# Kernel tuning notes

Hardware: AMD Instinct MI355X
Metric: run time of the kernel (lower is better)

## Reference

```python
import jax, jax.numpy as jnp
import numpy as np

SCALING = 32.0 / 16.0  # alpha / rank


def _nf4_levels():
    # q_i = Phi^{-1}((i+0.5)/16), normalized to [-1, 1]
    i = jnp.arange(16, dtype=jnp.float32)
    p = jnp.clip((i + 0.5) / 16.0, 1e-6, 1.0 - 1e-6)
    lv = jnp.sqrt(2.0) * jax.scipy.special.erfinv(2.0 * p - 1.0)
    return lv / jnp.max(jnp.abs(lv))


def _dequantize(q_weight, scales):
    # q_weight: (out, in//2) packed nibbles; scales: (out, num_groups)
    out_f, packed = q_weight.shape
    in_f = packed * 2
    hi = (q_weight >> 4) & 15
    lo = q_weight & 15
    idx = jnp.stack([hi, lo], axis=-1).reshape(out_f, in_f)  # interleave hi/lo
    w = _nf4_levels()[idx]  # (out, in)
    num_groups = scales.shape[1]
    block = in_f // num_groups
    w = (w.reshape(out_f, num_groups, block) * scales[:, :, None].astype(jnp.float32))
    return w.reshape(out_f, in_f)


def setup_inputs() -> dict:
    key = jax.random.key(0)
    k1, k2, k3, k4, k5 = jax.random.split(key, 5)
    B, S, IN, OUT, R, BLK = 4, 64, 8192, 8192, 16, 64
    x = jax.random.normal(k1, (B, S, IN), dtype=jnp.float32)
    q_weight = jax.random.randint(k2, (OUT, IN // 2), 0, 256, dtype=jnp.int32)
    scales = jax.random.uniform(k3, (OUT, IN // BLK), dtype=jnp.float32) * 0.02 + 1e-4
    lora_A = jax.random.normal(k4, (R, IN), dtype=jnp.float32) * 0.02
    lora_B = jax.random.normal(k5, (OUT, R), dtype=jnp.float32) * 0.02
    return {"x": x, "q_weight": q_weight, "scales": scales,
            "lora_A": lora_A, "lora_B": lora_B}


def reference(x, q_weight, scales, lora_A, lora_B):
    w = _dequantize(q_weight, scales)               # (out, in) fp32
    base = jnp.einsum('bsi,oi->bso', x, w)          # F.linear(x, W)
    lora = jnp.einsum('bsi,ri->bsr', x, lora_A)     # x @ A^T (dropout p=0)
    lora = jnp.einsum('bsr,or->bso', lora, lora_B)  # @ B^T
    return base + SCALING * lora
```

## Files before the change

kernel.cpp:

```cpp
#include <hip/hip_runtime.h>
#include <hip/hip_bf16.h>
#include <stdint.h>

typedef __attribute__((ext_vector_type(4))) float f32x4;
typedef __attribute__((ext_vector_type(8))) short short8;
typedef __attribute__((ext_vector_type(4))) int int4v;

#define IN_F   8192
#define OUT_F  8192
#define MROWS  256
#define BN     128
#define BK     64
#define NGRP   128

__device__ unsigned short g_xb[MROWS * IN_F];
__device__ float          g_t[MROWS * 16];
__device__ float          g_part[4 * MROWS * OUT_F];

__device__ __constant__ float NF4_LVL[16] = {
  -1.0f,        -0.70756721f, -0.54221982f, -0.41681853f,
  -0.31090474f, -0.21594601f, -0.12734085f, -0.04209530f,
   0.04209530f,  0.12734085f,  0.21594601f,  0.31090474f,
   0.41681853f,  0.54221982f,  0.70756721f,  1.0f };

static __device__ inline uint32_t pkbf(float a, float b) {
  __bf16 ha = (__bf16)a, hb = (__bf16)b;
  return (uint32_t)__builtin_bit_cast(unsigned short, ha)
       | ((uint32_t)__builtin_bit_cast(unsigned short, hb) << 16);
}

__global__ __launch_bounds__(256) void k_convert(const float* __restrict__ x) {
  int cid = blockIdx.x * 256 + threadIdx.x;
  int kt = cid >> 11;
  int r  = (cid >> 3) & 255;
  int c  = cid & 7;
  const float* src = x + (size_t)r * IN_F + kt * 64 + c * 8;
  f32x4 v0 = *(const f32x4*)src;
  f32x4 v1 = *(const f32x4*)(src + 4);
  int4v ov;
  ov[0] = (int)pkbf(v0.x, v0.y); ov[1] = (int)pkbf(v0.z, v0.w);
  ov[2] = (int)pkbf(v1.x, v1.y); ov[3] = (int)pkbf(v1.z, v1.w);
  *(int4v*)(g_xb + (size_t)kt * 16384 + r * 64 + ((c ^ (r & 7)) << 3)) = ov;
}

__global__ __launch_bounds__(256) void k_xa(const float* __restrict__ x,
                                            const float* __restrict__ lora_A) {
  int m = blockIdx.x, tid = threadIdx.x;
  float acc[16];
#pragma unroll
  for (int r = 0; r < 16; ++r) acc[r] = 0.f;
  const float* xr = x + (size_t)m * IN_F;
  for (int it = 0; it < 8; ++it) {
    int k = (tid + it * 256) * 4;
    f32x4 xv = *(const f32x4*)(xr + k);
#pragma unroll
    for (int r = 0; r < 16; ++r) {
      f32x4 av = *(const f32x4*)(lora_A + (size_t)r * IN_F + k);
      acc[r] += xv.x * av.x + xv.y * av.y + xv.z * av.z + xv.w * av.w;
    }
  }
#pragma unroll
  for (int r = 0; r < 16; ++r) {
    float v = acc[r];
#pragma unroll
    for (int off = 32; off; off >>= 1) v += __shfl_xor(v, off, 64);
    acc[r] = v;
  }
  __shared__ float sm[4][16];
  int lane = tid & 63, wave = tid >> 6;
  if (lane == 0) {
#pragma unroll
    for (int r = 0; r < 16; ++r) sm[wave][r] = acc[r];
  }
  __syncthreads();
  if (tid < 16)
    g_t[m * 16 + tid] = 2.0f * (sm[0][tid] + sm[1][tid] + sm[2][tid] + sm[3][tid]);
}

__global__ __launch_bounds__(512, 2) void k_gemm(
    const int* __restrict__ qw, const float* __restrict__ scales)
{
  __shared__ unsigned short Al[2][MROWS * BK];
  __shared__ unsigned short Bl[2][BN * BK];
  __shared__ float lut16[16];

  int tid = threadIdx.x;
  int lane = tid & 63, wave = tid >> 6;
  if (tid < 16) lut16[tid] = NF4_LVL[tid];
  __syncthreads();

  int flat = blockIdx.y * 64 + blockIdx.x;
  int wg = (flat & 7) * 32 + (flat >> 3);
  int bx = wg & 63, bz = wg >> 6;
  int n0 = bx * BN;
  int ktg0 = bz * 32;

  int n_0 = tid >> 3, c_0 = tid & 7;
  int n_1 = n_0 + 64;
  const int* qr0 = qw + (size_t)(n0 + n_0) * (IN_F / 2) + c_0 * 4;
  const int* qr1 = qw + (size_t)(n0 + n_1) * (IN_F / 2) + c_0 * 4;
  const float* sr0 = scales + (size_t)(n0 + n_0) * NGRP;
  const float* sr1 = scales + (size_t)(n0 + n_1) * NGRP;
  int boff0 = n_0 * 128 + ((c_0 ^ (n_0 & 7)) << 4);
  int boff1 = boff0 + 64 * 128;

  f32x4 acc[4][4];
#pragma unroll
  for (int i = 0; i < 4; ++i)
#pragma unroll
    for (int j = 0; j < 4; ++j) acc[i][j] = (f32x4){0.f, 0.f, 0.f, 0.f};

  int wr = wave >> 1, wc = wave & 1;
  int wm = wr * 64, wn = wc * 64;

  auto stageA = [&](int buf, int kt) {
    const char* src = (const char*)g_xb + (size_t)kt * 32768 + tid * 16;
    char* dst = (char*)(&Al[buf][0]) + tid * 16;
#pragma unroll
    for (int j = 0; j < 4; ++j)
      __builtin_amdgcn_global_load_lds(
          (const __attribute__((address_space(1))) void*)(src + j * 8192),
          (__attribute__((address_space(3))) void*)(dst + j * 8192), 16, 0, 0);
  };

  auto dqst = [&](int buf, int4v q0, float s0, int4v q1, float s1) {
    char* Bb = (char*)(&Bl[buf][0]);
    int4v ov;
#pragma unroll
    for (int e = 0; e < 4; ++e) {
      float hi = lut16[(q0[e] >> 4) & 15];
      float lo = lut16[q0[e] & 15];
      ov[e] = (int)pkbf(hi * s0, lo * s0);
    }
    *(int4v*)(Bb + boff0) = ov;
#pragma unroll
    for (int e = 0; e < 4; ++e) {
      float hi = lut16[(q1[e] >> 4) & 15];
      float lo = lut16[q1[e] & 15];
      ov[e] = (int)pkbf(hi * s1, lo * s1);
    }
    *(int4v*)(Bb + boff1) = ov;
  };

  auto compute = [&](int buf) {
    const char* Ab = (const char*)(&Al[buf][0]);
    const char* Bb = (const char*)(&Bl[buf][0]);
#pragma unroll
    for (int kk = 0; kk < 2; ++kk) {
      short8 af[4], bfv[4];
#pragma unroll
      for (int mi = 0; mi < 4; ++mi) {
        int r = wm + mi * 16 + (lane & 15);
        int cch = (kk * 4 + (lane >> 4)) ^ (r & 7);
        af[mi] = *(const short8*)(Ab + r * 128 + cch * 16);
      }
#pragma unroll
      for (int ni = 0; ni < 4; ++ni) {
        int n = wn + ni * 16 + (lane & 15);
        int cch = (kk * 4 + (lane >> 4)) ^ (n & 7);
        bfv[ni] = *(const short8*)(Bb + n * 128 + cch * 16);
      }
      __builtin_amdgcn_s_setprio(1);
#pragma unroll
      for (int mi = 0; mi < 4; ++mi)
#pragma unroll
        for (int ni = 0; ni < 4; ++ni)
          acc[mi][ni] = __builtin_amdgcn_mfma_f32_16x16x32_bf16(
              af[mi], bfv[ni], acc[mi][ni], 0, 0, 0);
      __builtin_amdgcn_s_setprio(0);
    }
  };

  int4v qa0 = *(const int4v*)(qr0 + ktg0 * 32);
  int4v qa1 = *(const int4v*)(qr1 + ktg0 * 32);
  float sa0 = sr0[ktg0], sa1 = sr1[ktg0];
  stageA(0, ktg0);
  int4v qb0 = *(const int4v*)(qr0 + (ktg0 + 1) * 32);
  int4v qb1 = *(const int4v*)(qr1 + (ktg0 + 1) * 32);
  float sb0 = sr0[ktg0 + 1], sb1 = sr1[ktg0 + 1];
  dqst(0, qa0, sa0, qa1, sa1);
  asm volatile("s_waitcnt vmcnt(0) lgkmcnt(0)" ::: "memory");
  __builtin_amdgcn_s_barrier();

  for (int t = 0; t < 31; ++t) {
    int c = t & 1;
    int kn = ktg0 + ((t < 30) ? (t + 2) : 0);
    int4v qn0 = *(const int4v*)(qr0 + kn * 32);
    int4v qn1 = *(const int4v*)(qr1 + kn * 32);
    float sn0 = sr0[kn], sn1 = sr1[kn];
    stageA(c ^ 1, ktg0 + t + 1);
    dqst(c ^ 1, qb0, sb0, qb1, sb1);
    compute(c);
    asm volatile("s_waitcnt vmcnt(0) lgkmcnt(0)" ::: "memory");
    __builtin_amdgcn_s_barrier();
    qb0 = qn0; qb1 = qn1; sb0 = sn0; sb1 = sn1;
  }
  compute(1);

  float* op = g_part + (size_t)bz * MROWS * OUT_F;
#pragma unroll
  for (int mi = 0; mi < 4; ++mi) {
#pragma unroll
    for (int ni = 0; ni < 4; ++ni) {
      int m = wm + mi * 16 + (lane >> 4) * 4;
      int nn = n0 + wn + ni * 16 + (lane & 15);
#pragma unroll
      for (int j = 0; j < 4; ++j)
        op[(size_t)(m + j) * OUT_F + nn] = acc[mi][ni][j];
    }
  }
}

__global__ __launch_bounds__(256) void k_reduce(const float* __restrict__ lora_B,
                                                float* __restrict__ out) {
  size_t i = ((size_t)blockIdx.x * 256 + threadIdx.x) * 4;
  int m = (int)(i >> 13);
  int n = (int)(i & 8191);
  f32x4 v = *(const f32x4*)(g_part + i);
  v += *(const f32x4*)(g_part + (size_t)1 * MROWS * OUT_F + i);
  v += *(const f32x4*)(g_part + (size_t)2 * MROWS * OUT_F + i);
  v += *(const f32x4*)(g_part + (size_t)3 * MROWS * OUT_F + i);
  const float* tr = g_t + m * 16;
  f32x4 t0 = *(const f32x4*)tr,       t1 = *(const f32x4*)(tr + 4);
  f32x4 t2 = *(const f32x4*)(tr + 8), t3 = *(const f32x4*)(tr + 12);
#pragma unroll
  for (int j = 0; j < 4; ++j) {
    const float* br = lora_B + (size_t)(n + j) * 16;
    f32x4 b0 = *(const f32x4*)br,       b1 = *(const f32x4*)(br + 4);
    f32x4 b2 = *(const f32x4*)(br + 8), b3 = *(const f32x4*)(br + 12);
    v[j] += t0.x*b0.x + t0.y*b0.y + t0.z*b0.z + t0.w*b0.w
          + t1.x*b1.x + t1.y*b1.y + t1.z*b1.z + t1.w*b1.w
          + t2.x*b2.x + t2.y*b2.y + t2.z*b2.z + t2.w*b2.w
          + t3.x*b3.x + t3.y*b3.y + t3.z*b3.z + t3.w*b3.w;
  }
  *(f32x4*)(out + i) = v;
}

extern "C" void kernel_launch(void* const* d_in, const int* in_sizes, int n_in,
                              void* d_out, int out_size, void* d_ws, size_t ws_size,
                              hipStream_t stream) {
  const float* x  = (const float*)d_in[0];
  const int*   qw = (const int*)d_in[1];
  const float* sc = (const float*)d_in[2];
  const float* lA = (const float*)d_in[3];
  const float* lB = (const float*)d_in[4];
  float* out = (float*)d_out;

  k_convert<<<1024, 256, 0, stream>>>(x);
  k_xa<<<256, 256, 0, stream>>>(x, lA);
  k_gemm<<<dim3(64, 4), 512, 0, stream>>>(qw, sc);
  k_reduce<<<2048, 256, 0, stream>>>(lB, out);
}
```

Before: 107.5 us.

## Pre-swizzle activations into MFMA fragment order and read them directly from global

k_convert now writes the bf16 activations in the exact per-lane MFMA fragment order, so the GEMM loads A operands straight from global (L2) into registers and drops the LDS staging of A. The N tile is halved to 64, giving 512 workgroups with launch bounds of 4 per CU, and LDS holds only the dequantized B tile. Dequantization uses a 256-entry LUT of packed bf16 pairs, so one lookup covers both nibbles of a byte. The intent is to cut LDS traffic and footprint and to raise occupancy and parallelism, at the cost of more redundant global reads of A across N tiles and higher latency on those A loads.

Result: no change. 107.1 us (-0.3%).

```diff
diff --git a/kernel.cpp b/kernel.cpp
--- a/kernel.cpp
+++ b/kernel.cpp
@@ -9,9 +9,10 @@
 #define IN_F   8192
 #define OUT_F  8192
 #define MROWS  256
-#define BN     128
+#define BN     64
 #define BK     64
 #define NGRP   128
+#define KTILES 32
 
 __device__ unsigned short g_xb[MROWS * IN_F];
 __device__ float          g_t[MROWS * 16];
@@ -30,17 +31,18 @@
 }
 
 __global__ __launch_bounds__(256) void k_convert(const float* __restrict__ x) {
-  int cid = blockIdx.x * 256 + threadIdx.x;
-  int kt = cid >> 11;
-  int r  = (cid >> 3) & 255;
-  int c  = cid & 7;
-  const float* src = x + (size_t)r * IN_F + kt * 64 + c * 8;
+  int d = blockIdx.x * 256 + threadIdx.x;
+  int l15 = d & 15, sub = (d >> 4) & 3, kk = (d >> 6) & 1;
+  int m16 = (d >> 7) & 15, kt = d >> 11;
+  int r = m16 * 16 + l15;
+  int k = kt * 64 + (kk * 4 + sub) * 8;
+  const float* src = x + (size_t)r * IN_F + k;
   f32x4 v0 = *(const f32x4*)src;
   f32x4 v1 = *(const f32x4*)(src + 4);
   int4v ov;
   ov[0] = (int)pkbf(v0.x, v0.y); ov[1] = (int)pkbf(v0.z, v0.w);
   ov[2] = (int)pkbf(v1.x, v1.y); ov[3] = (int)pkbf(v1.z, v1.w);
-  *(int4v*)(g_xb + (size_t)kt * 16384 + r * 64 + ((c ^ (r & 7)) << 3)) = ov;
+  *(int4v*)(g_xb + (size_t)d * 8) = ov;
 }
 
 __global__ __launch_bounds__(256) void k_xa(const float* __restrict__ x,
@@ -77,133 +79,141 @@
     g_t[m * 16 + tid] = 2.0f * (sm[0][tid] + sm[1][tid] + sm[2][tid] + sm[3][tid]);
 }
 
-__global__ __launch_bounds__(512, 2) void k_gemm(
+__global__ __launch_bounds__(512, 4) void k_gemm(
     const int* __restrict__ qw, const float* __restrict__ scales)
 {
-  __shared__ unsigned short Al[2][MROWS * BK];
   __shared__ unsigned short Bl[2][BN * BK];
-  __shared__ float lut16[16];
+  __shared__ uint32_t lut2[256];
 
   int tid = threadIdx.x;
   int lane = tid & 63, wave = tid >> 6;
-  if (tid < 16) lut16[tid] = NF4_LVL[tid];
+  if (tid < 256) lut2[tid] = pkbf(NF4_LVL[tid >> 4], NF4_LVL[tid & 15]);
+
+  int flat = blockIdx.x;
+  int wg = (flat & 7) * 64 + (flat >> 3);
+  int bx = wg & 127, bz = wg >> 7;
+  int n0 = bx * BN;
+  int ktg0 = bz * KTILES;
+
+  int dn = tid >> 3, dc = tid & 7;
+  const int* qr = qw + (size_t)(n0 + dn) * (IN_F / 2) + dc * 4;
+  const float* sr = scales + (size_t)(n0 + dn) * NGRP;
+  int boff = dn * 128 + ((dc ^ (dn & 7)) << 4);
+
+  f32x4 acc[4][2];
+#pragma unroll
+  for (int i = 0; i < 4; ++i)
+#pragma unroll
+    for (int j = 0; j < 2; ++j) acc[i][j] = (f32x4){0.f, 0.f, 0.f, 0.f};
+
+  int wr = wave >> 1, wc = wave & 1;
+  int wn = wc * 32;
+  int sub = lane >> 4, l15 = lane & 15;
+
+  int aoff = (wr * 4) * 1024 + (sub * 16 + l15) * 8;
+
+  auto dqst = [&](int buf, int4v q, float s) {
+    int4v ov;
+#pragma unroll
+    for (int e = 0; e < 4; ++e) {
+      uint32_t pk = lut2[q[e] & 255];
+      float fh = __builtin_bit_cast(float, pk << 16);
+      float fl = __builtin_bit_cast(float, pk & 0xFFFF0000u);
+      ov[e] = (int)pkbf(fh * s, fl * s);
+    }
+    *(int4v*)((char*)(&Bl[buf][0]) + boff) = ov;
+  };
+
   __syncthreads();
 
-  int flat = blockIdx.y * 64 + blockIdx.x;
-  int wg = (flat & 7) * 32 + (flat >> 3);
-  int bx = wg & 63, bz = wg >> 6;
-  int n0 = bx * BN;
-  int ktg0 = bz * 32;
-
-  int n_0 = tid >> 3, c_0 = tid & 7;
-  int n_1 = n_0 + 64;
-  const int* qr0 = qw + (size_t)(n0 + n_0) * (IN_F / 2) + c_0 * 4;
-  const int* qr1 = qw + (size_t)(n0 + n_1) * (IN_F / 2) + c_0 * 4;
-  const float* sr0 = scales + (size_t)(n0 + n_0) * NGRP;
-  const float* sr1 = scales + (size_t)(n0 + n_1) * NGRP;
-  int boff0 = n_0 * 128 + ((c_0 ^ (n_0 & 7)) << 4);
-  int boff1 = boff0 + 64 * 128;
-
-  f32x4 acc[4][4];
-#pragma unroll
-  for (int i = 0; i < 4; ++i)
-#pragma unroll
-    for (int j = 0; j < 4; ++j) acc[i][j] = (f32x4){0.f, 0.f, 0.f, 0.f};
-
-  int wr = wave >> 1, wc = wave & 1;
-  int wm = wr * 64, wn = wc * 64;
-
-  auto stageA = [&](int buf, int kt) {
-    const char* src = (const char*)g_xb + (size_t)kt * 32768 + tid * 16;
-    char* dst = (char*)(&Al[buf][0]) + tid * 16;
-#pragma unroll
-    for (int j = 0; j < 4; ++j)
-      __builtin_amdgcn_global_load_lds(
-          (const __attribute__((address_space(1))) void*)(src + j * 8192),
-          (__attribute__((address_space(3))) void*)(dst + j * 8192), 16, 0, 0);
-  };
-
-  auto dqst = [&](int buf, int4v q0, float s0, int4v q1, float s1) {
-    char* Bb = (char*)(&Bl[buf][0]);
-    int4v ov;
-#pragma unroll
-    for (int e = 0; e < 4; ++e) {
-      float hi = lut16[(q0[e] >> 4) & 15];
-      float lo = lut16[q0[e] & 15];
-      ov[e] = (int)pkbf(hi * s0, lo * s0);
-    }
-    *(int4v*)(Bb + boff0) = ov;
-#pragma unroll
-    for (int e = 0; e < 4; ++e) {
-      float hi = lut16[(q1[e] >> 4) & 15];
-      float lo = lut16[q1[e] & 15];
-      ov[e] = (int)pkbf(hi * s1, lo * s1);
-    }
-    *(int4v*)(Bb + boff1) = ov;
-  };
-
-  auto compute = [&](int buf) {
-    const char* Ab = (const char*)(&Al[buf][0]);
-    const char* Bb = (const char*)(&Bl[buf][0]);
-#pragma unroll
-    for (int kk = 0; kk < 2; ++kk) {
-      short8 af[4], bfv[4];
-#pragma unroll
-      for (int mi = 0; mi < 4; ++mi) {
-        int r = wm + mi * 16 + (lane & 15);
-        int cch = (kk * 4 + (lane >> 4)) ^ (r & 7);
-        af[mi] = *(const short8*)(Ab + r * 128 + cch * 16);
+  int4v qcur = *(const int4v*)(qr + ktg0 * 32);
+  float scur = sr[ktg0];
+  dqst(0, qcur, scur);
+  int4v qnxt = *(const int4v*)(qr + (ktg0 + 1) * 32);
+  float snxt = sr[ktg0 + 1];
+  asm volatile("s_waitcnt lgkmcnt(0)" ::: "memory");
+  __builtin_amdgcn_s_barrier();
+
+  for (int t = 0; t < KTILES - 1; ++t) {
+    int cur = t & 1;
+    int ktg = ktg0 + t;
+
+    short8 bfv[2][2];
+#pragma unroll
+    for (int kk = 0; kk < 2; ++kk)
+#pragma unroll
+      for (int ni = 0; ni < 2; ++ni) {
+        int n = wn + ni * 16 + l15;
+        int cch = (kk * 4 + sub) ^ (n & 7);
+        bfv[kk][ni] = *(const short8*)((const char*)(&Bl[cur][0]) + n * 128 + cch * 16);
       }
-#pragma unroll
-      for (int ni = 0; ni < 4; ++ni) {
-        int n = wn + ni * 16 + (lane & 15);
-        int cch = (kk * 4 + (lane >> 4)) ^ (n & 7);
-        bfv[ni] = *(const short8*)(Bb + n * 128 + cch * 16);
+
+    short8 af[2][4];
+    const unsigned short* ab = g_xb + (size_t)ktg * 16384;
+#pragma unroll
+    for (int kk = 0; kk < 2; ++kk)
+#pragma unroll
+      for (int mi = 0; mi < 4; ++mi)
+        af[kk][mi] = *(const short8*)(ab + aoff + mi * 1024 + kk * 512);
+
+    int kn = (t < KTILES - 2) ? (ktg0 + t + 2) : (ktg0 + KTILES - 1);
+    int4v qn2 = *(const int4v*)(qr + kn * 32);
+    float sn2 = sr[kn];
+
+    dqst(cur ^ 1, qnxt, snxt);
+    qnxt = qn2; snxt = sn2;
+
+    __builtin_amdgcn_s_setprio(1);
+#pragma unroll
+    for (int kk = 0; kk < 2; ++kk)
+#pragma unroll
+      for (int mi = 0; mi < 4; ++mi)
+#pragma unroll
+        for (int ni = 0; ni < 2; ++ni)
+          acc[mi][ni] = __builtin_amdgcn_mfma_f32_16x16x32_bf16(
+              af[kk][mi], bfv[kk][ni], acc[mi][ni], 0, 0, 0);
+    __builtin_amdgcn_s_setprio(0);
+
+    asm volatile("s_waitcnt lgkmcnt(0)" ::: "memory");
+    __builtin_amdgcn_s_barrier();
+  }
+
+  {
+    int cur = (KTILES - 1) & 1;
+    int ktg = ktg0 + KTILES - 1;
+    short8 bfv[2][2];
+#pragma unroll
+    for (int kk = 0; kk < 2; ++kk)
+#pragma unroll
+      for (int ni = 0; ni < 2; ++ni) {
+        int n = wn + ni * 16 + l15;
+        int cch = (kk * 4 + sub) ^ (n & 7);
+        bfv[kk][ni] = *(const short8*)((const char*)(&Bl[cur][0]) + n * 128 + cch * 16);
       }
-      __builtin_amdgcn_s_setprio(1);
-#pragma unroll
-      for (int mi = 0; mi < 4; ++mi)
-#pragma unroll
-        for (int ni = 0; ni < 4; ++ni)
+    short8 af[2][4];
+    const unsigned short* ab = g_xb + (size_t)ktg * 16384;
+#pragma unroll
+    for (int kk = 0; kk < 2; ++kk)
+#pragma unroll
+      for (int mi = 0; mi < 4; ++mi)
+        af[kk][mi] = *(const short8*)(ab + aoff + mi * 1024 + kk * 512);
+#pragma unroll
+    for (int kk = 0; kk < 2; ++kk)
+#pragma unroll
+      for (int mi = 0; mi < 4; ++mi)
+#pragma unroll
+        for (int ni = 0; ni < 2; ++ni)
           acc[mi][ni] = __builtin_amdgcn_mfma_f32_16x16x32_bf16(
-              af[mi], bfv[ni], acc[mi][ni], 0, 0, 0);
-      __builtin_amdgcn_s_setprio(0);
-    }
-  };
-
-  int4v qa0 = *(const int4v*)(qr0 + ktg0 * 32);
-  int4v qa1 = *(const int4v*)(qr1 + ktg0 * 32);
-  float sa0 = sr0[ktg0], sa1 = sr1[ktg0];
-  stageA(0, ktg0);
-  int4v qb0 = *(const int4v*)(qr0 + (ktg0 + 1) * 32);
-  int4v qb1 = *(const int4v*)(qr1 + (ktg0 + 1) * 32);
-  float sb0 = sr0[ktg0 + 1], sb1 = sr1[ktg0 + 1];
-  dqst(0, qa0, sa0, qa1, sa1);
-  asm volatile("s_waitcnt vmcnt(0) lgkmcnt(0)" ::: "memory");
-  __builtin_amdgcn_s_barrier();
-
-  for (int t = 0; t < 31; ++t) {
-    int c = t & 1;
-    int kn = ktg0 + ((t < 30) ? (t + 2) : 0);
-    int4v qn0 = *(const int4v*)(qr0 + kn * 32);
-    int4v qn1 = *(const int4v*)(qr1 + kn * 32);
-    float sn0 = sr0[kn], sn1 = sr1[kn];
-    stageA(c ^ 1, ktg0 + t + 1);
-    dqst(c ^ 1, qb0, sb0, qb1, sb1);
-    compute(c);
-    asm volatile("s_waitcnt vmcnt(0) lgkmcnt(0)" ::: "memory");
-    __builtin_amdgcn_s_barrier();
-    qb0 = qn0; qb1 = qn1; sb0 = sn0; sb1 = sn1;
-  }
-  compute(1);
+              af[kk][mi], bfv[kk][ni], acc[mi][ni], 0, 0, 0);
+  }
 
   float* op = g_part + (size_t)bz * MROWS * OUT_F;
 #pragma unroll
   for (int mi = 0; mi < 4; ++mi) {
 #pragma unroll
-    for (int ni = 0; ni < 4; ++ni) {
-      int m = wm + mi * 16 + (lane >> 4) * 4;
-      int nn = n0 + wn + ni * 16 + (lane & 15);
+    for (int ni = 0; ni < 2; ++ni) {
+      int m = wr * 64 + mi * 16 + sub * 4;
+      int nn = n0 + wn + ni * 16 + l15;
 #pragma unroll
       for (int j = 0; j < 4; ++j)
         op[(size_t)(m + j) * OUT_F + nn] = acc[mi][ni][j];
@@ -248,6 +258,6 @@
 
   k_convert<<<1024, 256, 0, stream>>>(x);
   k_xa<<<256, 256, 0, stream>>>(x, lA);
-  k_gemm<<<dim3(64, 4), 512, 0, stream>>>(qw, sc);
+  k_gemm<<<512, 512, 0, stream>>>(qw, sc);
   k_reduce<<<2048, 256, 0, stream>>>(lB, out);
 }
```
